# Optimization experiments

Hardware: AMD Instinct MI355X
Metric: run time of the kernel (lower is better)

The kernel has to match this reference:

```python
import jax, jax.numpy as jnp
import numpy as np

B, S, IN = 4096, 2048, 8
H, LIN, A = 8, 4, 4

def _lstm_cell(x, h, c, Wih, Whh, bih, bhh):
    # torch gate order: i, f, g, o ; gates: [B, 4H]
    gates = x @ Wih.T + h @ Whh.T + bih + bhh
    i, f, g, o = jnp.split(gates, 4, axis=-1)
    i = jax.nn.sigmoid(i); f = jax.nn.sigmoid(f)
    g = jnp.tanh(g);       o = jax.nn.sigmoid(o)
    c = f * c + i * g
    h = o * jnp.tanh(c)
    return h, c

def setup_inputs() -> dict:
    key = jax.random.key(0)
    ks = jax.random.split(key, 20)
    seq = jax.random.normal(ks[0], (B, S, IN), dtype=jnp.float32)
    lengths = jax.random.randint(ks[1], (B,), 1, S + 1, dtype=jnp.int32)
    def w(k, shape, scale=0.1):
        return (jax.random.normal(k, shape, dtype=jnp.float32) * scale)
    return {
        "seq": seq, "lengths": lengths,
        # LSTM layer 0 (input 8 -> hidden 8)
        "Wih0": w(ks[2], (4 * H, IN)), "Whh0": w(ks[3], (4 * H, H)),
        "bih0": w(ks[4], (4 * H,)),   "bhh0": w(ks[5], (4 * H,)),
        # LSTM layer 1 (hidden 8 -> hidden 8)
        "Wih1": w(ks[6], (4 * H, H)), "Whh1": w(ks[7], (4 * H, H)),
        "bih1": w(ks[8], (4 * H,)),  "bhh1": w(ks[9], (4 * H,)),
        # heads
        "Wl": w(ks[10], (LIN, H)),  "bl": w(ks[11], (LIN,)),
        "Wv": w(ks[12], (1, LIN)),  "bv": jnp.zeros((1,), jnp.float32),
        "Wa": w(ks[13], (A, LIN)),  "ba": jnp.zeros((A,), jnp.float32),
        "log_std": jnp.zeros((1, A), jnp.float32),
    }

def reference(seq, lengths, Wih0, Whh0, bih0, bhh0, Wih1, Whh1, bih1, bhh1,
              Wl, bl, Wv, bv, Wa, ba, log_std):
    b = seq.shape[0]
    xs = jnp.transpose(seq, (1, 0, 2))  # [S, B, IN] time-major for scan
    z = jnp.zeros((b, H), seq.dtype)

    def step(carry, x_t):
        h0, c0, h1, c1 = carry
        h0, c0 = _lstm_cell(x_t, h0, c0, Wih0, Whh0, bih0, bhh0)
        h1, c1 = _lstm_cell(h0, h1, c1, Wih1, Whh1, bih1, bhh1)
        return (h0, c0, h1, c1), h1

    _, outs = jax.lax.scan(step, (z, z, z, z), xs)  # outs: [S, B, H]
    # packed-sequence semantics: take the last VALID output per sequence
    y = outs[lengths - 1, jnp.arange(b)]            # [B, H]
    feat = jnp.tanh(y @ Wl.T + bl)                  # [B, LIN]
    value = feat @ Wv.T + bv                        # [B, 1]
    action_mean = feat @ Wa.T + ba                  # [B, A]
    action_log_std = jnp.broadcast_to(log_std, action_mean.shape)
    action_std = jnp.exp(action_log_std)
    return value, action_mean, action_log_std, action_std
```

## Files before the change

### kernel.cpp

```cpp
#include <hip/hip_runtime.h>

#define B_ 4096
#define S_ 2048
#define CH 16

typedef float v2f __attribute__((ext_vector_type(2)));

__device__ __forceinline__ float rcp_(float x)  { return __builtin_amdgcn_rcpf(x); }
__device__ __forceinline__ float exp2_(float x) { return __builtin_amdgcn_exp2f(x); }
__device__ __forceinline__ float tanh_(float x) {
    return fmaf(-2.0f, rcp_(1.0f + exp2_(2.88539008f * x)), 1.0f);
}
template<int CTRL>
__device__ __forceinline__ float dppf(float x) {
    int v = __builtin_bit_cast(int, x);
    return __builtin_bit_cast(float,
        __builtin_amdgcn_update_dpp(v, v, CTRL, 0xF, 0xF, false));
}
__device__ __forceinline__ int dppi_ror2(int x) {
    return __builtin_amdgcn_update_dpp(x, x, 0x122, 0xF, 0xF, false);
}
__device__ __forceinline__ void ld8(const float* p, float* o) {
    float4 a = *(const float4*)p;
    float4 b = *(const float4*)(p + 4);
    o[0] = a.x; o[1] = a.y; o[2] = a.z; o[3] = a.w;
    o[4] = b.x; o[5] = b.y; o[6] = b.z; o[7] = b.w;
}

#define L2E 1.44269504f

__global__ __launch_bounds__(768) void lstm_main(
    const float* __restrict__ seq, const int* __restrict__ lengths,
    const float* __restrict__ Wih0, const float* __restrict__ Whh0,
    const float* __restrict__ bih0, const float* __restrict__ bhh0,
    const float* __restrict__ Wih1, const float* __restrict__ Whh1,
    const float* __restrict__ bih1, const float* __restrict__ bhh1,
    const float* __restrict__ Wl, const float* __restrict__ bl,
    const float* __restrict__ Wv, const float* __restrict__ bv,
    const float* __restrict__ Wa, const float* __restrict__ ba,
    const float* __restrict__ lstd, float* __restrict__ out)
{
    __shared__ float  ring0[2][CH][128];
    __shared__ float4 ringX[2][CH][16][8];
    __shared__ float4 ringY[2][CH][16][8];

    const int tid = threadIdx.x;
    const int wv  = tid >> 6;
    const int l   = tid & 63;
    const int p   = l & 1;
    const int j   = (l >> 1) & 7;
    const int s8  = (l >> 4) * 2 + p;

    const bool heavy = (wv % 3) == 0;
    int layer, sbase, s0 = 0;
    if (heavy) {
        const int hid = wv / 3;
        layer = hid >> 1;
        sbase = (hid & 1) * 8;
    } else {
        layer = (wv >= 7) ? 1 : 0;
        const int idx = (layer == 0) ? ((wv >= 4) ? (wv - 2) : (wv - 1))
                                     : ((wv >= 10) ? (wv - 8) : (wv - 7));
        sbase = (idx >> 1) * 8;
        s0    = (idx & 1) * 8;
    }
    const int sq = sbase + s8;
    const int b  = blockIdx.x * 16 + sq;

    const int probe = dppi_ror2(j);
    const int delta = (j - probe) & 7;

    v2f wA[8], wB[8];
    v2f biasA = (v2f){0.0f, 0.0f}, biasB = (v2f){0.0f, 0.0f};
    if (heavy) {
        const float* Whh = layer ? Whh1 : Whh0;
        int idx = j;
        #pragma unroll
        for (int k = 0; k < 8; ++k) {
            wA[k] = (v2f){ Whh[(j)      * 8 + idx] * -L2E,
                           Whh[(8 + j)  * 8 + idx] * -L2E };
            wB[k] = (v2f){ Whh[(16 + j) * 8 + idx] * (2.0f * L2E),
                           Whh[(24 + j) * 8 + idx] * -L2E };
            idx = (idx - delta) & 7;
        }
    } else {
        const float* Wih = layer ? Wih1 : Wih0;
        const float* bi  = layer ? bih1 : bih0;
        const float* bh  = layer ? bhh1 : bhh0;
        #pragma unroll
        for (int k = 0; k < 8; ++k) {
            wA[k] = (v2f){ Wih[(j)      * 8 + k] * -L2E,
                           Wih[(8 + j)  * 8 + k] * -L2E };
            wB[k] = (v2f){ Wih[(16 + j) * 8 + k] * (2.0f * L2E),
                           Wih[(24 + j) * 8 + k] * -L2E };
        }
        biasA = (v2f){ (bi[j]      + bh[j])      * -L2E,
                       (bi[8 + j]  + bh[8 + j])  * -L2E };
        biasB = (v2f){ (bi[16 + j] + bh[16 + j]) * (2.0f * L2E),
                       (bi[24 + j] + bh[24 + j]) * -L2E };
    }

    int m = lengths[blockIdx.x * 16 + (l & 15)];
    m = max(m, __shfl_xor(m, 1));
    m = max(m, __shfl_xor(m, 2));
    m = max(m, __shfl_xor(m, 4));
    m = max(m, __shfl_xor(m, 8));
    const int nch   = (m + CH - 1) / CH;
    const int lenm1 = lengths[b] - 1;

    float hq = 0.0f, cq = 0.0f, ysave = 0.0f;
    const float* xbase = seq + (size_t)b * S_ * 8;

    if (heavy) __builtin_amdgcn_s_setprio(1);

    auto rstep = [&](v2f aA, v2f aB) {
        const float r0 = hq;
        const float r1 = dppf<0x122>(hq);
        const float r2 = dppf<0x124>(hq);
        const float r3 = dppf<0x126>(hq);
        const float r4 = dppf<0x128>(hq);
        const float r5 = dppf<0x12A>(hq);
        const float r6 = dppf<0x12C>(hq);
        const float r7 = dppf<0x12E>(hq);
        v2f aA1, aB1;
        aA  += wA[0] * (v2f){r0, r0};
        aB  += wB[0] * (v2f){r0, r0};
        aA1  = wA[4] * (v2f){r4, r4};
        aB1  = wB[4] * (v2f){r4, r4};
        aA  += wA[1] * (v2f){r1, r1};
        aB  += wB[1] * (v2f){r1, r1};
        aA1 += wA[5] * (v2f){r5, r5};
        aB1 += wB[5] * (v2f){r5, r5};
        aA  += wA[2] * (v2f){r2, r2};
        aB  += wB[2] * (v2f){r2, r2};
        aA1 += wA[6] * (v2f){r6, r6};
        aB1 += wB[6] * (v2f){r6, r6};
        aA  += wA[3] * (v2f){r3, r3};
        aB  += wB[3] * (v2f){r3, r3};
        aA1 += wA[7] * (v2f){r7, r7};
        aB1 += wB[7] * (v2f){r7, r7};
        aA += aA1; aB += aB1;
        float Ei = exp2_(aA.x), Ef = exp2_(aA.y);
        float Eg = exp2_(aB.x), Eo = exp2_(aB.y);
        float pi = 1.0f + Ei, pf = 1.0f + Ef;
        float pg = 1.0f + Eg, po = 1.0f + Eo;
        float P  = pi * pg;
        float T  = P * pf;
        float R  = rcp_(T * po);
        float sf  = (R * P) * po;
        float itg = ((Eg - 1.0f) * (R * pf)) * po;
        cq = fmaf(sf, cq, itg);
        float so = R * T;
        hq = so * tanh_(cq);
    };

    for (int k = 0; k <= nch + 2; ++k) {
        if (!heavy) {
            if (layer == 0) {
                if (k < nch) {
                    const int t0 = k * CH + s0;
                    float xv[8][8];
                    #pragma unroll
                    for (int s = 0; s < 8; ++s)
                        ld8(xbase + (size_t)(t0 + s) * 8, xv[s]);
                    #pragma unroll
                    for (int s = 0; s < 8; ++s) {
                        v2f aA = biasA, aB = biasB;
                        #pragma unroll
                        for (int q = 0; q < 8; ++q) {
                            aA += wA[q] * (v2f){xv[s][q], xv[s][q]};
                            aB += wB[q] * (v2f){xv[s][q], xv[s][q]};
                        }
                        ringX[k & 1][s0 + s][sq][j] = make_float4(aA.x, aA.y, aB.x, aB.y);
                    }
                }
            } else {
                const int c = k - 2;
                if (c >= 0 && c < nch) {
                    #pragma unroll
                    for (int s = 0; s < 8; ++s) {
                        const float4 ha = *(const float4*)&ring0[c & 1][s0 + s][sq * 8];
                        const float4 hb = *(const float4*)&ring0[c & 1][s0 + s][sq * 8 + 4];
                        float hv[8] = {ha.x, ha.y, ha.z, ha.w, hb.x, hb.y, hb.z, hb.w};
                        v2f aA = biasA, aB = biasB;
                        #pragma unroll
                        for (int q = 0; q < 8; ++q) {
                            aA += wA[q] * (v2f){hv[q], hv[q]};
                            aB += wB[q] * (v2f){hv[q], hv[q]};
                        }
                        ringY[c & 1][s0 + s][sq][j] = make_float4(aA.x, aA.y, aB.x, aB.y);
                    }
                }
            }
        } else if (layer == 0) {
            const int c = k - 1;
            if (c >= 0 && c < nch) {
                float4 xg[CH];
                #pragma unroll
                for (int s = 0; s < CH; ++s) xg[s] = ringX[c & 1][s][sq][j];
                float* r0p = &ring0[c & 1][0][sq * 8 + j];
                #pragma unroll
                for (int s = 0; s < CH; ++s) {
                    rstep((v2f){xg[s].x, xg[s].y}, (v2f){xg[s].z, xg[s].w});
                    r0p[s * 128] = hq;
                }
            }
        } else {
            const int c = k - 3;
            if (c >= 0 && c < nch) {
                float4 yg[CH];
                #pragma unroll
                for (int s = 0; s < CH; ++s) yg[s] = ringY[c & 1][s][sq][j];
                const int u0 = c * CH;
                #pragma unroll
                for (int s = 0; s < CH; ++s) {
                    rstep((v2f){yg[s].x, yg[s].y}, (v2f){yg[s].z, yg[s].w});
                    ysave = (u0 + s == lenm1) ? hq : ysave;
                }
            }
        }
        __syncthreads();
    }

    if (heavy && layer == 1) {
        const int lbase = (l & 48) | p;
        float yv[8];
        #pragma unroll
        for (int k = 0; k < 8; ++k) yv[k] = __shfl(ysave, lbase + 2 * k);
        if (j == 0) {
            float feat[4];
            #pragma unroll
            for (int q = 0; q < 4; ++q) {
                float acc = bl[q];
                #pragma unroll
                for (int k = 0; k < 8; ++k) acc = fmaf(Wl[q * 8 + k], yv[k], acc);
                feat[q] = tanh_(acc);
            }
            float val = bv[0];
            #pragma unroll
            for (int q = 0; q < 4; ++q) val = fmaf(Wv[q], feat[q], val);
            out[b] = val;
            #pragma unroll
            for (int a = 0; a < 4; ++a) {
                float am = ba[a];
                #pragma unroll
                for (int q = 0; q < 4; ++q) am = fmaf(Wa[a * 4 + q], feat[q], am);
                out[4096  + b * 4 + a] = am;
                float ls = lstd[a];
                out[20480 + b * 4 + a] = ls;
                out[36864 + b * 4 + a] = exp2_(L2E * ls);
            }
        }
    }
}

extern "C" void kernel_launch(void* const* d_in, const int* in_sizes, int n_in,
                              void* d_out, int out_size, void* d_ws, size_t ws_size,
                              hipStream_t stream)
{
    const float* seq   = (const float*)d_in[0];
    const int* lengths = (const int*)d_in[1];
    const float* Wih0  = (const float*)d_in[2];
    const float* Whh0  = (const float*)d_in[3];
    const float* bih0  = (const float*)d_in[4];
    const float* bhh0  = (const float*)d_in[5];
    const float* Wih1  = (const float*)d_in[6];
    const float* Whh1  = (const float*)d_in[7];
    const float* bih1  = (const float*)d_in[8];
    const float* bhh1  = (const float*)d_in[9];
    const float* Wl    = (const float*)d_in[10];
    const float* bl    = (const float*)d_in[11];
    const float* Wv    = (const float*)d_in[12];
    const float* bv    = (const float*)d_in[13];
    const float* Wa    = (const float*)d_in[14];
    const float* ba    = (const float*)d_in[15];
    const float* lstd  = (const float*)d_in[16];

    lstm_main<<<B_ / 16, 768, 0, stream>>>(seq, lengths, Wih0, Whh0, bih0, bhh0,
                                           Wih1, Whh1, bih1, bhh1,
                                           Wl, bl, Wv, bv, Wa, ba, lstd,
                                           (float*)d_out);
}
```

Measured before the change: 646.8 us.

## Replace block-wide barriers with per-group LDS counter handshakes between pipeline stages

Replaces the per-chunk __syncthreads lockstep across all 12 waves with fine-grained producer/consumer counters in shared memory, kept per 8-sequence group. Each stage waits only on the counters it depends on, using spin-waits with s_sleep. The trip count now comes from the max length within the group rather than across all 16 sequences, so groups with shorter sequences stop earlier. This removes barrier stalls and lets stages drift apart, at the cost of spin polling and reliance on LDS memory-ordering correctness.

```diff
diff --git a/kernel.cpp b/kernel.cpp
--- a/kernel.cpp
+++ b/kernel.cpp
@@ -43,6 +43,7 @@
     __shared__ float  ring0[2][CH][128];
     __shared__ float4 ringX[2][CH][16][8];
     __shared__ float4 ringY[2][CH][16][8];
+    volatile __shared__ int ctr[2][9];
 
     const int tid = threadIdx.x;
     const int wv  = tid >> 6;
@@ -51,8 +52,14 @@
     const int j   = (l >> 1) & 7;
     const int s8  = (l >> 4) * 2 + p;
 
+    {
+        volatile int* cf = &ctr[0][0];
+        if (tid < 18) cf[tid] = 0;
+    }
+    __syncthreads();
+
     const bool heavy = (wv % 3) == 0;
-    int layer, sbase, s0 = 0;
+    int layer, sbase, s0 = 0, ph = 0;
     if (heavy) {
         const int hid = wv / 3;
         layer = hid >> 1;
@@ -62,9 +69,11 @@
         const int idx = (layer == 0) ? ((wv >= 4) ? (wv - 2) : (wv - 1))
                                      : ((wv >= 10) ? (wv - 8) : (wv - 7));
         sbase = (idx >> 1) * 8;
-        s0    = (idx & 1) * 8;
+        ph    = idx & 1;
+        s0    = ph * 8;
     }
     const int sq = sbase + s8;
+    const int g  = sbase >> 3;
     const int b  = blockIdx.x * 16 + sq;
 
     const int probe = dppi_ror2(j);
@@ -100,16 +109,20 @@
                        (bi[24 + j] + bh[24 + j]) * -L2E };
     }
 
-    int m = lengths[blockIdx.x * 16 + (l & 15)];
+    int m = lengths[b];
     m = max(m, __shfl_xor(m, 1));
-    m = max(m, __shfl_xor(m, 2));
-    m = max(m, __shfl_xor(m, 4));
-    m = max(m, __shfl_xor(m, 8));
-    const int nch   = (m + CH - 1) / CH;
+    m = max(m, __shfl_xor(m, 16));
+    m = max(m, __shfl_xor(m, 32));
+    const int nchw  = (m + CH - 1) / CH;
     const int lenm1 = lengths[b] - 1;
 
     float hq = 0.0f, cq = 0.0f, ysave = 0.0f;
     const float* xbase = seq + (size_t)b * S_ * 8;
+
+    auto waitge = [&](int idx, int want) {
+        while (ctr[g][idx] < want) __builtin_amdgcn_s_sleep(2);
+        __threadfence_block();
+    };
 
     if (heavy) __builtin_amdgcn_s_setprio(1);
 
@@ -154,75 +167,84 @@
         hq = so * tanh_(cq);
     };
 
-    for (int k = 0; k <= nch + 2; ++k) {
-        if (!heavy) {
-            if (layer == 0) {
-                if (k < nch) {
-                    const int t0 = k * CH + s0;
-                    float xv[8][8];
-                    #pragma unroll
-                    for (int s = 0; s < 8; ++s)
-                        ld8(xbase + (size_t)(t0 + s) * 8, xv[s]);
-                    #pragma unroll
-                    for (int s = 0; s < 8; ++s) {
-                        v2f aA = biasA, aB = biasB;
-                        #pragma unroll
-                        for (int q = 0; q < 8; ++q) {
-                            aA += wA[q] * (v2f){xv[s][q], xv[s][q]};
-                            aB += wB[q] * (v2f){xv[s][q], xv[s][q]};
-                        }
-                        ringX[k & 1][s0 + s][sq][j] = make_float4(aA.x, aA.y, aB.x, aB.y);
-                    }
+    if (!heavy && layer == 0) {
+        for (int k = 0; k < nchw; ++k) {
+            waitge(2, k - 1);
+            const int t0 = k * CH + s0;
+            float xv[8][8];
+            #pragma unroll
+            for (int s = 0; s < 8; ++s)
+                ld8(xbase + (size_t)(t0 + s) * 8, xv[s]);
+            #pragma unroll
+            for (int s = 0; s < 8; ++s) {
+                v2f aA = biasA, aB = biasB;
+                #pragma unroll
+                for (int q = 0; q < 8; ++q) {
+                    aA += wA[q] * (v2f){xv[s][q], xv[s][q]};
+                    aB += wB[q] * (v2f){xv[s][q], xv[s][q]};
                 }
-            } else {
-                const int c = k - 2;
-                if (c >= 0 && c < nch) {
-                    #pragma unroll
-                    for (int s = 0; s < 8; ++s) {
-                        const float4 ha = *(const float4*)&ring0[c & 1][s0 + s][sq * 8];
-                        const float4 hb = *(const float4*)&ring0[c & 1][s0 + s][sq * 8 + 4];
-                        float hv[8] = {ha.x, ha.y, ha.z, ha.w, hb.x, hb.y, hb.z, hb.w};
-                        v2f aA = biasA, aB = biasB;
-                        #pragma unroll
-                        for (int q = 0; q < 8; ++q) {
-                            aA += wA[q] * (v2f){hv[q], hv[q]};
-                            aB += wB[q] * (v2f){hv[q], hv[q]};
-                        }
-                        ringY[c & 1][s0 + s][sq][j] = make_float4(aA.x, aA.y, aB.x, aB.y);
-                    }
+                ringX[k & 1][s0 + s][sq][j] = make_float4(aA.x, aA.y, aB.x, aB.y);
+            }
+            __threadfence_block();
+            if (l == 0) ctr[g][ph] = k + 1;
+        }
+    } else if (!heavy) {
+        for (int n = 0; n < nchw; ++n) {
+            waitge(3, n + 1);
+            waitge(8, n - 1);
+            #pragma unroll
+            for (int s = 0; s < 8; ++s) {
+                const float4 ha = *(const float4*)&ring0[n & 1][s0 + s][sq * 8];
+                const float4 hb = *(const float4*)&ring0[n & 1][s0 + s][sq * 8 + 4];
+                float hv[8] = {ha.x, ha.y, ha.z, ha.w, hb.x, hb.y, hb.z, hb.w};
+                v2f aA = biasA, aB = biasB;
+                #pragma unroll
+                for (int q = 0; q < 8; ++q) {
+                    aA += wA[q] * (v2f){hv[q], hv[q]};
+                    aB += wB[q] * (v2f){hv[q], hv[q]};
                 }
-            }
-        } else if (layer == 0) {
-            const int c = k - 1;
-            if (c >= 0 && c < nch) {
-                float4 xg[CH];
-                #pragma unroll
-                for (int s = 0; s < CH; ++s) xg[s] = ringX[c & 1][s][sq][j];
-                float* r0p = &ring0[c & 1][0][sq * 8 + j];
-                #pragma unroll
-                for (int s = 0; s < CH; ++s) {
-                    rstep((v2f){xg[s].x, xg[s].y}, (v2f){xg[s].z, xg[s].w});
-                    r0p[s * 128] = hq;
-                }
-            }
-        } else {
-            const int c = k - 3;
-            if (c >= 0 && c < nch) {
-                float4 yg[CH];
-                #pragma unroll
-                for (int s = 0; s < CH; ++s) yg[s] = ringY[c & 1][s][sq][j];
-                const int u0 = c * CH;
-                #pragma unroll
-                for (int s = 0; s < CH; ++s) {
-                    rstep((v2f){yg[s].x, yg[s].y}, (v2f){yg[s].z, yg[s].w});
-                    ysave = (u0 + s == lenm1) ? hq : ysave;
-                }
-            }
-        }
-        __syncthreads();
-    }
-
-    if (heavy && layer == 1) {
+                ringY[n & 1][s0 + s][sq][j] = make_float4(aA.x, aA.y, aB.x, aB.y);
+            }
+            __threadfence_block();
+            if (l == 0) { ctr[g][4 + ph] = n + 1;
+                          ctr[g][6 + ph] = n + 1; }
+        }
+    } else if (layer == 0) {
+        for (int c = 0; c < nchw; ++c) {
+            waitge(0, c + 1);
+            waitge(1, c + 1);
+            float4 xg[CH];
+            #pragma unroll
+            for (int s = 0; s < CH; ++s) xg[s] = ringX[c & 1][s][sq][j];
+            __threadfence_block();
+            if (l == 0) ctr[g][2] = c + 1;
+            waitge(4, c - 1);
+            waitge(5, c - 1);
+            float* r0p = &ring0[c & 1][0][sq * 8 + j];
+            #pragma unroll
+            for (int s = 0; s < CH; ++s) {
+                rstep((v2f){xg[s].x, xg[s].y}, (v2f){xg[s].z, xg[s].w});
+                r0p[s * 128] = hq;
+            }
+            __threadfence_block();
+            if (l == 0) ctr[g][3] = c + 1;
+        }
+    } else {
+        for (int c = 0; c < nchw; ++c) {
+            waitge(6, c + 1);
+            waitge(7, c + 1);
+            float4 yg[CH];
+            #pragma unroll
+            for (int s = 0; s < CH; ++s) yg[s] = ringY[c & 1][s][sq][j];
+            __threadfence_block();
+            if (l == 0) ctr[g][8] = c + 1;
+            const int u0 = c * CH;
+            #pragma unroll
+            for (int s = 0; s < CH; ++s) {
+                rstep((v2f){yg[s].x, yg[s].y}, (v2f){yg[s].z, yg[s].w});
+                ysave = (u0 + s == lenm1) ? hq : ysave;
+            }
+        }
         const int lbase = (l & 48) | p;
         float yv[8];
         #pragma unroll
```

After: 698.8 us. 1.08x slower.
